# Optimization experiments

Measured on AMD Instinct MI355X. Metric: run time of the kernel, lower is better.

The kernel has to match this reference:

```python
import jax, jax.numpy as jnp
import numpy as np

S, B, D, N, DH = 2048, 2, 1024, 16, 64  # seq, batch, d_model, n_head, d_head
LN_EPS = 1e-5


def setup_inputs() -> dict:
    key = jax.random.key(0)
    ks = jax.random.split(key, 8)
    h = jax.random.normal(ks[0], (S, B, D), dtype=jnp.float32)
    Wq = jax.random.normal(ks[1], (D, N * DH), dtype=jnp.float32) * 0.02
    Wkv = jax.random.normal(ks[2], (D, 2 * N * DH), dtype=jnp.float32) * 0.02
    Wo = jax.random.normal(ks[3], (N * DH, D), dtype=jnp.float32) * 0.02
    ln_gamma = jnp.ones((D,), dtype=jnp.float32)
    ln_beta = jnp.zeros((D,), dtype=jnp.float32)
    # persistent compressive-memory state from a previous segment
    memory = jax.random.normal(ks[4], (B, N, DH, DH), dtype=jnp.float32)
    # normalization is a sum of (elu(k)+1) over ~S positions -> strictly positive, O(S)
    mem_norm = jax.random.uniform(ks[5], (B, 1, N, DH), dtype=jnp.float32) * S + 1.0
    gate_beta = jnp.ones((1,), dtype=jnp.float32) * 0.01  # beta_eps
    return {"h": h, "Wq": Wq, "Wkv": Wkv, "Wo": Wo, "ln_gamma": ln_gamma,
            "ln_beta": ln_beta, "memory": memory, "mem_norm": mem_norm,
            "gate_beta": gate_beta}


def reference(h, Wq, Wkv, Wo, ln_gamma, ln_beta, memory, mem_norm, gate_beta):
    scale = 1.0 / np.sqrt(DH).astype(np.float32)
    # projections (pre_lnorm=False, mems=None -> c == h)
    q = (h @ Wq).reshape(S, B, N, DH)
    k, v = jnp.split(h @ Wkv, 2, axis=-1)
    k = k.reshape(S, B, N, DH)
    v = v.reshape(S, B, N, DH)
    # local quadratic attention
    score = jnp.einsum('ibnd,jbnd->ijbn', q, k) * scale  # [S,S,B,N]
    prob = jax.nn.softmax(score, axis=1)
    attn_vec = jnp.einsum('ijbn,jbnd->ibnd', prob, v).reshape(S, B, N * DH)
    # memory retrieval (NOTE: source swaps K/V in the _update_memory call;
    # it is done under no_grad -> stop_gradient here)
    cached_Q = jax.nn.elu(q.swapaxes(0, 1)) + 1.0          # [B,S,N,DH]
    num = jnp.einsum('bsnk,bnkv->bsnv', cached_Q, memory)   # [B,S,N,DH]
    den = jnp.einsum('bsnk,bvnk->bsnv', cached_Q, mem_norm)  # [B,S,N,1]
    content_A = jax.lax.stop_gradient(num / den)            # [B,S,N,DH]
    # gated injection
    g = jax.nn.sigmoid(gate_beta)                           # [1]
    inj = g * content_A.swapaxes(0, 1).reshape(S, B, N * DH) + (1.0 - g) * attn_vec
    attn_out = inj @ Wo
    # post layernorm residual
    y = h + attn_out
    mu = jnp.mean(y, axis=-1, keepdims=True)
    var = jnp.mean((y - mu) ** 2, axis=-1, keepdims=True)
    return (y - mu) / jnp.sqrt(var + LN_EPS) * ln_gamma + ln_beta
```

## Files before the change

### kernel.cpp

```cpp
#include <hip/hip_runtime.h>


typedef unsigned short ushort_t;
typedef unsigned int uint32;

typedef __bf16 bf16x8 __attribute__((ext_vector_type(8)));
typedef float f32x4 __attribute__((ext_vector_type(4)));
typedef float f32x16 __attribute__((ext_vector_type(16)));
typedef unsigned short u16x8 __attribute__((ext_vector_type(8)));
typedef unsigned short u16x4 __attribute__((ext_vector_type(4)));
typedef unsigned int u32x4 __attribute__((ext_vector_type(4)));

typedef const __attribute__((address_space(1))) void gvoid_t;
typedef __attribute__((address_space(3))) void lvoid_t;

#define S_LEN 2048
#define BATCH 2
#define NHEAD 16

__device__ __forceinline__ ushort_t f2bf(float x) {
  union { float f; unsigned u; } c; c.f = x;
  unsigned r = (c.u + 0x7FFFu + ((c.u >> 16) & 1u)) >> 16;
  return (ushort_t)r;
}
__device__ __forceinline__ float bf2f(ushort_t v) {
  union { unsigned u; float f; } c; c.u = ((unsigned)v) << 16;
  return c.f;
}

__global__ __launch_bounds__(256) void k_cvt_h(const float* __restrict__ src,
                                               ushort_t* __restrict__ dst, int n4) {
  int idx = blockIdx.x * 256 + threadIdx.x;
  if (idx >= n4) return;
  float4 v = ((const float4*)src)[idx];
  u16x4 o; o[0] = f2bf(v.x); o[1] = f2bf(v.y); o[2] = f2bf(v.z); o[3] = f2bf(v.w);
  ((u16x4*)dst)[idx] = o;
}

__global__ __launch_bounds__(256) void k_cvt_wT(const float* __restrict__ W,
                                                ushort_t* __restrict__ WT, int K, int N) {
  __shared__ float tile[32][33];
  const int n0 = blockIdx.x * 32, k0 = blockIdx.y * 32;
  const int tx = threadIdx.x & 31, ty = threadIdx.x >> 5;
#pragma unroll
  for (int r = 0; r < 32; r += 8)
    tile[ty + r][tx] = W[(size_t)(k0 + ty + r) * N + n0 + tx];
  __syncthreads();
#pragma unroll
  for (int r = 0; r < 32; r += 8)
    WT[(size_t)(n0 + ty + r) * K + k0 + tx] = f2bf(tile[tx][ty + r]);
}

template <int OUT_BF16>
__global__ __launch_bounds__(256) void k_gemm_bt(const ushort_t* __restrict__ A,
                                                 const ushort_t* __restrict__ B,
                                                 void* __restrict__ Cv, int M, int N, int K,
                                                 int nbx) {
  __shared__ __attribute__((aligned(16))) ushort_t As[128 * 32];
  __shared__ __attribute__((aligned(16))) ushort_t Bs[128 * 32];
  const int per = gridDim.x >> 3;
  const int fl = (blockIdx.x & 7) * per + (blockIdx.x >> 3);
  const int m0 = (fl / nbx) * 128, n0 = (fl % nbx) * 128;
  const int tid = threadIdx.x, w = tid >> 6, lane = tid & 63;
  const int wm = (w >> 1) * 64, wn = (w & 1) * 64;
  const int l15 = lane & 15, l4 = lane >> 4;
  f32x4 acc[4][4];
#pragma unroll
  for (int i = 0; i < 4; ++i)
#pragma unroll
    for (int j = 0; j < 4; ++j)
#pragma unroll
      for (int r = 0; r < 4; ++r) acc[i][j][r] = 0.f;

  for (int k0 = 0; k0 < K; k0 += 32) {
    __syncthreads();
#pragma unroll
    for (int r = 0; r < 2; ++r) {
      int c = r * 256 + w * 64 + lane;
      const ushort_t* ga = A + (size_t)(m0 + (c >> 2)) * K + k0 + (c & 3) * 8;
      const ushort_t* gb = B + (size_t)(n0 + (c >> 2)) * K + k0 + (c & 3) * 8;
      __builtin_amdgcn_global_load_lds((gvoid_t*)ga, (lvoid_t*)(As + (r * 256 + w * 64) * 8), 16, 0, 0);
      __builtin_amdgcn_global_load_lds((gvoid_t*)gb, (lvoid_t*)(Bs + (r * 256 + w * 64) * 8), 16, 0, 0);
    }
    __syncthreads();
    bf16x8 af[4], bfr[4];
#pragma unroll
    for (int i = 0; i < 4; ++i) af[i] = *(const bf16x8*)&As[(wm + i * 16 + l15) * 32 + l4 * 8];
#pragma unroll
    for (int j = 0; j < 4; ++j) bfr[j] = *(const bf16x8*)&Bs[(wn + j * 16 + l15) * 32 + l4 * 8];
#pragma unroll
    for (int i = 0; i < 4; ++i)
#pragma unroll
      for (int j = 0; j < 4; ++j)
        acc[i][j] = __builtin_amdgcn_mfma_f32_16x16x32_bf16(af[i], bfr[j], acc[i][j], 0, 0, 0);
  }
#pragma unroll
  for (int i = 0; i < 4; ++i)
#pragma unroll
    for (int j = 0; j < 4; ++j)
#pragma unroll
      for (int r = 0; r < 4; ++r) {
        int row = m0 + wm + i * 16 + l4 * 4 + r;
        int col = n0 + wn + j * 16 + l15;
        if (OUT_BF16)
          ((ushort_t*)Cv)[(size_t)row * N + col] = f2bf(acc[i][j][r]);
        else
          ((float*)Cv)[(size_t)row * N + col] = acc[i][j][r];
      }
}

__device__ __forceinline__ void stage_k(const ushort_t* __restrict__ qkv, ushort_t* kw,
                                        int j0, int b, int n, int w, int lane) {
#pragma unroll
  for (int r = 0; r < 2; ++r) {
    int jb_ = w * 16 + r * 8;
    const ushort_t* ksrc = qkv + (size_t)(j0 + jb_ + (lane >> 3)) * 6144 + b * 3072 + n * 64 + 1024
                           + (((lane & 7) ^ (lane >> 3)) << 3);
    __builtin_amdgcn_global_load_lds((gvoid_t*)ksrc, (lvoid_t*)(kw + jb_ * 64), 16, 0, 0);
  }
}

__global__ __launch_bounds__(256) void k_attn(const ushort_t* __restrict__ qkv,
                                              const float* __restrict__ mem,
                                              const float* __restrict__ mnorm,
                                              const float* __restrict__ gbeta,
                                              ushort_t* __restrict__ inj) {
  __shared__ __attribute__((aligned(16))) ushort_t Ks[2][4096];
  __shared__ __attribute__((aligned(16))) ushort_t VTs[2][4096];
  __shared__ __attribute__((aligned(16))) ushort_t Ms[4096];
  const int bn = blockIdx.y, b = bn & 1, n = bn >> 1;
  const int tid = threadIdx.x, w = tid >> 6, lane = tid & 63;
  const int l31 = lane & 31, h = lane >> 5;
  const int qrow = blockIdx.x * 128 + w * 32 + l31;
  const size_t qoff = (size_t)qrow * 6144 + b * 3072 + n * 64;
  bf16x8 qf[4];
#pragma unroll
  for (int ks = 0; ks < 4; ++ks) qf[ks] = *(const bf16x8*)(qkv + qoff + ks * 16 + h * 8);

  const int vj = tid >> 2, vdq = (tid & 3) * 16, a2 = (tid & 3) * 2;
  const size_t vbase = (size_t)b * 3072 + n * 64 + 2048 + vdq;
  const int krd = l31 & 7;
  const int fv0 = (l31 & 7) ^ (l31 >> 3);
  const int fv1 = fv0 ^ 4;

  stage_k(qkv, Ks[0], 0, b, n, w, lane);
  u16x8 vr0 = *(const u16x8*)(qkv + (size_t)vj * 6144 + vbase);
  u16x8 vr1 = *(const u16x8*)(qkv + (size_t)vj * 6144 + vbase + 8);
  {
    const float* mb = mem + (size_t)(b * NHEAD + n) * 4096;
#pragma unroll
    for (int r = 0; r < 4; ++r) {
      float4 mv = *(const float4*)(mb + tid * 16 + r * 4);
      u16x4 mo;
      mo[0] = f2bf(mv.x); mo[1] = f2bf(mv.y); mo[2] = f2bf(mv.z); mo[3] = f2bf(mv.w);
      *(u16x4*)&Ms[tid * 16 + r * 4] = mo;
    }
  }
#pragma unroll
  for (int e = 0; e < 8; ++e) {
    int f0 = (e ^ a2) << 3;
    VTs[0][(vdq + e) * 64 + (vj ^ f0)] = vr0[e];
    VTs[0][(vdq + 8 + e) * 64 + (vj ^ f0 ^ 8)] = vr1[e];
  }
  __syncthreads();

  f32x16 oacc[2];
#pragma unroll
  for (int r = 0; r < 16; ++r) { oacc[0][r] = 0.f; oacc[1][r] = 0.f; }
  float m_run = -1e30f, l_run = 0.f;
  const float CEXP = 0.18033688011113723f;

  for (int t = 0; t < 32; ++t) {
    const ushort_t* Kb = Ks[t & 1];
    const ushort_t* Vb = VTs[t & 1];
    u16x8 nv0, nv1;
    if (t < 31) {
      stage_k(qkv, Ks[(t + 1) & 1], (t + 1) * 64, b, n, w, lane);
      const ushort_t* vsrc = qkv + (size_t)((t + 1) * 64 + vj) * 6144 + vbase;
      nv0 = *(const u16x8*)vsrc;
      nv1 = *(const u16x8*)(vsrc + 8);
    }
    f32x16 sv[2];
#pragma unroll
    for (int r = 0; r < 16; ++r) { sv[0][r] = 0.f; sv[1][r] = 0.f; }
    __builtin_amdgcn_s_setprio(1);
#pragma unroll
    for (int jb = 0; jb < 2; ++jb) {
      const int rb = (jb * 32 + l31) * 64;
#pragma unroll
      for (int ks = 0; ks < 4; ++ks) {
        bf16x8 kf = *(const bf16x8*)&Kb[rb + ((((ks << 1) | h) ^ krd) << 3)];
        sv[jb] = __builtin_amdgcn_mfma_f32_32x32x16_bf16(kf, qf[ks], sv[jb], 0, 0, 0);
      }
    }
    __builtin_amdgcn_s_setprio(0);
    float mx[16];
#pragma unroll
    for (int r = 0; r < 16; ++r) mx[r] = fmaxf(sv[0][r], sv[1][r]);
#pragma unroll
    for (int st = 8; st >= 1; st >>= 1)
#pragma unroll
      for (int r = 0; r < st; ++r) mx[r] = fmaxf(mx[r], mx[r + st]);
    float tmax = fmaxf(mx[0], __shfl_xor(mx[0], 32));
    if (!__all(tmax <= m_run + 60.0f)) {
      float mnew = fmaxf(m_run, tmax);
      float alpha = __builtin_amdgcn_exp2f((m_run - mnew) * CEXP);
      l_run *= alpha;
#pragma unroll
      for (int r = 0; r < 16; ++r) { oacc[0][r] *= alpha; oacc[1][r] *= alpha; }
      m_run = mnew;
    }
    float p[32];
    const float mc = m_run * CEXP;
#pragma unroll
    for (int jb = 0; jb < 2; ++jb)
#pragma unroll
      for (int r = 0; r < 16; ++r)
        p[jb * 16 + r] = __builtin_amdgcn_exp2f(fmaf(sv[jb][r], CEXP, -mc));
    float ls[16];
#pragma unroll
    for (int r = 0; r < 16; ++r) ls[r] = p[r] + p[16 + r];
#pragma unroll
    for (int st = 8; st >= 1; st >>= 1)
#pragma unroll
      for (int r = 0; r < st; ++r) ls[r] += ls[r + st];
    l_run += ls[0] + __shfl_xor(ls[0], 32);
#pragma unroll
    for (int ks = 0; ks < 4; ++ks) {
      const int jb = ks >> 1, q0 = (ks & 1) * 2;
      uint32 X0, X1, Y0, Y1;
      asm volatile("v_cvt_pk_bf16_f32 %0, %1, %2" : "=v"(X0) : "v"(p[jb * 16 + q0 * 4 + 0]), "v"(p[jb * 16 + q0 * 4 + 1]));
      asm volatile("v_cvt_pk_bf16_f32 %0, %1, %2" : "=v"(X1) : "v"(p[jb * 16 + q0 * 4 + 2]), "v"(p[jb * 16 + q0 * 4 + 3]));
      asm volatile("v_cvt_pk_bf16_f32 %0, %1, %2" : "=v"(Y0) : "v"(p[jb * 16 + (q0 + 1) * 4 + 0]), "v"(p[jb * 16 + (q0 + 1) * 4 + 1]));
      asm volatile("v_cvt_pk_bf16_f32 %0, %1, %2" : "=v"(Y1) : "v"(p[jb * 16 + (q0 + 1) * 4 + 2]), "v"(p[jb * 16 + (q0 + 1) * 4 + 3]));
      asm volatile("v_permlane32_swap_b32 %0, %1" : "+v"(X0), "+v"(Y0));
      asm volatile("v_permlane32_swap_b32 %0, %1" : "+v"(X1), "+v"(Y1));
      union { u32x4 u; bf16x8 v; } pf;
      pf.u[0] = X0; pf.u[1] = X1; pf.u[2] = Y0; pf.u[3] = Y1;
      bf16x8 vf0 = *(const bf16x8*)&Vb[l31 * 64 + ((((ks << 1) | h) ^ fv0) << 3)];
      bf16x8 vf1 = *(const bf16x8*)&Vb[(32 + l31) * 64 + ((((ks << 1) | h) ^ fv1) << 3)];
      __builtin_amdgcn_s_setprio(1);
      oacc[0] = __builtin_amdgcn_mfma_f32_32x32x16_bf16(vf0, pf.v, oacc[0], 0, 0, 0);
      oacc[1] = __builtin_amdgcn_mfma_f32_32x32x16_bf16(vf1, pf.v, oacc[1], 0, 0, 0);
      __builtin_amdgcn_s_setprio(0);
    }
    if (t < 31) {
      ushort_t* Vw = VTs[(t + 1) & 1];
#pragma unroll
      for (int e = 0; e < 8; ++e) {
        int f0 = (e ^ a2) << 3;
        Vw[(vdq + e) * 64 + (vj ^ f0)] = nv0[e];
        Vw[(vdq + 8 + e) * 64 + (vj ^ f0 ^ 8)] = nv1[e];
      }
      __syncthreads();
    }
  }

  float den = 0.f;
  bf16x8 cqf[4];
  const float* nrm = mnorm + (size_t)(b * NHEAD + n) * 64;
#pragma unroll
  for (int ks = 0; ks < 4; ++ks) {
    union { u16x8 u; bf16x8 v; } qv, cu;
    qv.v = qf[ks];
#pragma unroll
    for (int e = 0; e < 8; ++e) {
      float x = bf2f(qv.u[e]);
      float c = (x > 0.f) ? (x + 1.f) : __builtin_amdgcn_exp2f(x * 1.4426950408889634f);
      cu.u[e] = f2bf(c);
      den += c * nrm[ks * 16 + h * 8 + e];
    }
    cqf[ks] = cu.v;
  }
  den += __shfl_xor(den, 32);

  f32x16 accv[2];
#pragma unroll
  for (int r = 0; r < 16; ++r) { accv[0][r] = 0.f; accv[1][r] = 0.f; }
#pragma unroll
  for (int db = 0; db < 2; ++db)
#pragma unroll
    for (int ks = 0; ks < 4; ++ks) {
      union { u16x8 u; bf16x8 v; } af;
#pragma unroll
      for (int e = 0; e < 8; ++e)
        af.u[e] = Ms[(ks * 16 + h * 8 + e) * 64 + db * 32 + l31];
      accv[db] = __builtin_amdgcn_mfma_f32_32x32x16_bf16(af.v, cqf[ks], accv[db], 0, 0, 0);
    }

  float g = 1.f / (1.f + expf(-gbeta[0]));
  float rden = 1.f / den, invl = 1.f / l_run;
  ushort_t* op = inj + (size_t)qrow * 2048 + b * 1024 + n * 64;
#pragma unroll
  for (int db = 0; db < 2; ++db)
#pragma unroll
    for (int qq = 0; qq < 4; ++qq) {
      u16x4 st;
#pragma unroll
      for (int m = 0; m < 4; ++m) {
        float content = accv[db][qq * 4 + m] * rden;
        float av = oacc[db][qq * 4 + m] * invl;
        st[m] = f2bf(g * content + (1.f - g) * av);
      }
      *(u16x4*)(op + db * 32 + qq * 8 + h * 4) = st;
    }
}

__global__ __launch_bounds__(256) void k_ln(const float* __restrict__ h,
                                            const float* __restrict__ ao,
                                            const float* __restrict__ gam,
                                            const float* __restrict__ bet,
                                            float* __restrict__ out) {
  const int m = blockIdx.x, t = threadIdx.x;
  const int lane = t & 63, w = t >> 6;
  __shared__ float redS[4], redQ[4];
  const size_t base = (size_t)m * 1024;
  float4 hv = ((const float4*)(h + base))[t];
  float4 avv = ((const float4*)(ao + base))[t];
  float y0 = hv.x + avv.x, y1 = hv.y + avv.y, y2 = hv.z + avv.z, y3 = hv.w + avv.w;
  float s = y0 + y1 + y2 + y3;
  float sq = y0 * y0 + y1 * y1 + y2 * y2 + y3 * y3;
#pragma unroll
  for (int mk = 32; mk >= 1; mk >>= 1) { s += __shfl_xor(s, mk); sq += __shfl_xor(sq, mk); }
  if (lane == 0) { redS[w] = s; redQ[w] = sq; }
  __syncthreads();
  float Ssum = redS[0] + redS[1] + redS[2] + redS[3];
  float Qsum = redQ[0] + redQ[1] + redQ[2] + redQ[3];
  float mu = Ssum * (1.f / 1024.f);
  float var = Qsum * (1.f / 1024.f) - mu * mu;
  float rstd = rsqrtf(var + 1e-5f);
  float4 g = ((const float4*)gam)[t];
  float4 bt = ((const float4*)bet)[t];
  float4 o;
  o.x = (y0 - mu) * rstd * g.x + bt.x;
  o.y = (y1 - mu) * rstd * g.y + bt.y;
  o.z = (y2 - mu) * rstd * g.z + bt.z;
  o.w = (y3 - mu) * rstd * g.w + bt.w;
  ((float4*)(out + base))[t] = o;
}

extern "C" void kernel_launch(void* const* d_in, const int* in_sizes, int n_in,
                              void* d_out, int out_size, void* d_ws, size_t ws_size,
                              hipStream_t stream) {
  const float* h = (const float*)d_in[0];
  const float* Wq = (const float*)d_in[1];
  const float* Wkv = (const float*)d_in[2];
  const float* Wo = (const float*)d_in[3];
  const float* gam = (const float*)d_in[4];
  const float* bet = (const float*)d_in[5];
  const float* mem = (const float*)d_in[6];
  const float* mnorm = (const float*)d_in[7];
  const float* gbeta = (const float*)d_in[8];
  float* out = (float*)d_out;

  char* ws = (char*)d_ws;
  ushort_t* hb  = (ushort_t*)(ws);
  ushort_t* wT  = (ushort_t*)(ws + (size_t)(8u << 20));
  ushort_t* woT = (ushort_t*)(ws + (size_t)(14u << 20));
  ushort_t* qkv = (ushort_t*)(ws + (size_t)(16u << 20));
  float*    ao  = (float*)   (ws + (size_t)(16u << 20));
  ushort_t* inj = hb;

  k_cvt_h<<<4096, 256, 0, stream>>>(h, hb, 1048576);
  k_cvt_wT<<<dim3(32, 32), 256, 0, stream>>>(Wq, wT, 1024, 1024);
  k_cvt_wT<<<dim3(64, 32), 256, 0, stream>>>(Wkv, wT + (size_t)1024 * 1024, 1024, 2048);
  k_cvt_wT<<<dim3(32, 32), 256, 0, stream>>>(Wo, woT, 1024, 1024);
  k_gemm_bt<1><<<768, 256, 0, stream>>>(hb, wT, (void*)qkv, 4096, 3072, 1024, 24);
  k_attn<<<dim3(16, 32), 256, 0, stream>>>(qkv, mem, mnorm, gbeta, inj);
  k_gemm_bt<0><<<256, 256, 0, stream>>>(inj, woT, (void*)ao, 4096, 1024, 1024, 8);
  k_ln<<<4096, 256, 0, stream>>>(h, ao, gam, bet, out);
}
```

Before: 155.8 us.

## Split attention KV range across two half-blocks and add 64-row output GEMM

The attention kernel now runs 512 threads per block. Each half processes 16 of the 32 key tiles, and the two partial softmax states are merged through shared memory, which doubles parallelism across the key dimension. The memory matrix is no longer staged in LDS; it is read straight from global memory and converted in the retrieval MFMA loop. The output projection moves to a new GEMM with 64x128 tiles and 512 blocks for better CU coverage. In exchange there is extra LDS traffic for the merge, idle threads in the upper half after the merge, and uncoalesced global reads of the memory matrix.

After: 169.2 us. +8.5%, slower.

```diff
diff --git a/kernel.cpp b/kernel.cpp
--- a/kernel.cpp
+++ b/kernel.cpp
@@ -109,6 +109,60 @@
       }
 }
 
+__global__ __launch_bounds__(256) void k_gemm64(const ushort_t* __restrict__ A,
+                                                const ushort_t* __restrict__ B,
+                                                float* __restrict__ C, int M, int N, int K,
+                                                int nbx) {
+  __shared__ __attribute__((aligned(16))) ushort_t As[64 * 32];
+  __shared__ __attribute__((aligned(16))) ushort_t Bs[128 * 32];
+  const int per = gridDim.x >> 3;
+  const int fl = (blockIdx.x & 7) * per + (blockIdx.x >> 3);
+  const int m0 = (fl / nbx) * 64, n0 = (fl % nbx) * 128;
+  const int tid = threadIdx.x, w = tid >> 6, lane = tid & 63;
+  const int wn = w * 32;
+  const int l15 = lane & 15, l4 = lane >> 4;
+  f32x4 acc[4][2];
+#pragma unroll
+  for (int i = 0; i < 4; ++i)
+#pragma unroll
+    for (int j = 0; j < 2; ++j)
+#pragma unroll
+      for (int r = 0; r < 4; ++r) acc[i][j][r] = 0.f;
+
+  for (int k0 = 0; k0 < K; k0 += 32) {
+    __syncthreads();
+    {
+      int c = w * 64 + lane;
+      const ushort_t* ga = A + (size_t)(m0 + (c >> 2)) * K + k0 + (c & 3) * 8;
+      __builtin_amdgcn_global_load_lds((gvoid_t*)ga, (lvoid_t*)(As + w * 512), 16, 0, 0);
+#pragma unroll
+      for (int r = 0; r < 2; ++r) {
+        int c2 = r * 256 + w * 64 + lane;
+        const ushort_t* gb = B + (size_t)(n0 + (c2 >> 2)) * K + k0 + (c2 & 3) * 8;
+        __builtin_amdgcn_global_load_lds((gvoid_t*)gb, (lvoid_t*)(Bs + r * 2048 + w * 512), 16, 0, 0);
+      }
+    }
+    __syncthreads();
+    bf16x8 af[4], bfr[2];
+#pragma unroll
+    for (int i = 0; i < 4; ++i) af[i] = *(const bf16x8*)&As[(i * 16 + l15) * 32 + l4 * 8];
+#pragma unroll
+    for (int j = 0; j < 2; ++j) bfr[j] = *(const bf16x8*)&Bs[(wn + j * 16 + l15) * 32 + l4 * 8];
+#pragma unroll
+    for (int i = 0; i < 4; ++i)
+#pragma unroll
+      for (int j = 0; j < 2; ++j)
+        acc[i][j] = __builtin_amdgcn_mfma_f32_16x16x32_bf16(af[i], bfr[j], acc[i][j], 0, 0, 0);
+  }
+#pragma unroll
+  for (int i = 0; i < 4; ++i)
+#pragma unroll
+    for (int j = 0; j < 2; ++j)
+#pragma unroll
+      for (int r = 0; r < 4; ++r)
+        C[(size_t)(m0 + i * 16 + l4 * 4 + r) * N + n0 + wn + j * 16 + l15] = acc[i][j][r];
+}
+
 __device__ __forceinline__ void stage_k(const ushort_t* __restrict__ qkv, ushort_t* kw,
                                         int j0, int b, int n, int w, int lane) {
 #pragma unroll
@@ -120,47 +174,43 @@
   }
 }
 
-__global__ __launch_bounds__(256) void k_attn(const ushort_t* __restrict__ qkv,
-                                              const float* __restrict__ mem,
-                                              const float* __restrict__ mnorm,
-                                              const float* __restrict__ gbeta,
-                                              ushort_t* __restrict__ inj) {
-  __shared__ __attribute__((aligned(16))) ushort_t Ks[2][4096];
-  __shared__ __attribute__((aligned(16))) ushort_t VTs[2][4096];
-  __shared__ __attribute__((aligned(16))) ushort_t Ms[4096];
+__global__ __launch_bounds__(512, 4) void k_attn(const ushort_t* __restrict__ qkv,
+                                                 const float* __restrict__ mem,
+                                                 const float* __restrict__ mnorm,
+                                                 const float* __restrict__ gbeta,
+                                                 ushort_t* __restrict__ inj) {
+  __shared__ __attribute__((aligned(16))) ushort_t smem[32768];
   const int bn = blockIdx.y, b = bn & 1, n = bn >> 1;
-  const int tid = threadIdx.x, w = tid >> 6, lane = tid & 63;
+  const int tid = threadIdx.x;
+  const int hh = tid >> 8;
+  const int ht = tid & 255;
+  const int w4 = (tid >> 6) & 3, lane = tid & 63;
   const int l31 = lane & 31, h = lane >> 5;
-  const int qrow = blockIdx.x * 128 + w * 32 + l31;
+  const int qrow = blockIdx.x * 128 + w4 * 32 + l31;
   const size_t qoff = (size_t)qrow * 6144 + b * 3072 + n * 64;
   bf16x8 qf[4];
 #pragma unroll
   for (int ks = 0; ks < 4; ++ks) qf[ks] = *(const bf16x8*)(qkv + qoff + ks * 16 + h * 8);
 
-  const int vj = tid >> 2, vdq = (tid & 3) * 16, a2 = (tid & 3) * 2;
+  const int vj = ht >> 2, vdq = (ht & 3) * 16, a2 = (ht & 3) * 2;
   const size_t vbase = (size_t)b * 3072 + n * 64 + 2048 + vdq;
   const int krd = l31 & 7;
   const int fv0 = (l31 & 7) ^ (l31 >> 3);
   const int fv1 = fv0 ^ 4;
-
-  stage_k(qkv, Ks[0], 0, b, n, w, lane);
-  u16x8 vr0 = *(const u16x8*)(qkv + (size_t)vj * 6144 + vbase);
-  u16x8 vr1 = *(const u16x8*)(qkv + (size_t)vj * 6144 + vbase + 8);
+  const int tile0 = hh * 16;
+
+  stage_k(qkv, smem + hh * 8192, tile0 * 64, b, n, w4, lane);
   {
-    const float* mb = mem + (size_t)(b * NHEAD + n) * 4096;
-#pragma unroll
-    for (int r = 0; r < 4; ++r) {
-      float4 mv = *(const float4*)(mb + tid * 16 + r * 4);
-      u16x4 mo;
-      mo[0] = f2bf(mv.x); mo[1] = f2bf(mv.y); mo[2] = f2bf(mv.z); mo[3] = f2bf(mv.w);
-      *(u16x4*)&Ms[tid * 16 + r * 4] = mo;
-    }
-  }
-#pragma unroll
-  for (int e = 0; e < 8; ++e) {
-    int f0 = (e ^ a2) << 3;
-    VTs[0][(vdq + e) * 64 + (vj ^ f0)] = vr0[e];
-    VTs[0][(vdq + 8 + e) * 64 + (vj ^ f0 ^ 8)] = vr1[e];
+    const ushort_t* vsrc = qkv + (size_t)(tile0 * 64 + vj) * 6144 + vbase;
+    u16x8 vr0 = *(const u16x8*)vsrc;
+    u16x8 vr1 = *(const u16x8*)(vsrc + 8);
+    ushort_t* Vw = smem + 16384 + hh * 8192;
+#pragma unroll
+    for (int e = 0; e < 8; ++e) {
+      int f0 = (e ^ a2) << 3;
+      Vw[(vdq + e) * 64 + (vj ^ f0)] = vr0[e];
+      Vw[(vdq + 8 + e) * 64 + (vj ^ f0 ^ 8)] = vr1[e];
+    }
   }
   __syncthreads();
 
@@ -170,13 +220,14 @@
   float m_run = -1e30f, l_run = 0.f;
   const float CEXP = 0.18033688011113723f;
 
-  for (int t = 0; t < 32; ++t) {
-    const ushort_t* Kb = Ks[t & 1];
-    const ushort_t* Vb = VTs[t & 1];
+  for (int t = 0; t < 16; ++t) {
+    const int bb = t & 1;
+    const ushort_t* Kb = smem + (hh * 2 + bb) * 4096;
+    const ushort_t* Vb = smem + 16384 + (hh * 2 + bb) * 4096;
     u16x8 nv0, nv1;
-    if (t < 31) {
-      stage_k(qkv, Ks[(t + 1) & 1], (t + 1) * 64, b, n, w, lane);
-      const ushort_t* vsrc = qkv + (size_t)((t + 1) * 64 + vj) * 6144 + vbase;
+    if (t < 15) {
+      stage_k(qkv, smem + (hh * 2 + (bb ^ 1)) * 4096, (tile0 + t + 1) * 64, b, n, w4, lane);
+      const ushort_t* vsrc = qkv + (size_t)((tile0 + t + 1) * 64 + vj) * 6144 + vbase;
       nv0 = *(const u16x8*)vsrc;
       nv1 = *(const u16x8*)(vsrc + 8);
     }
@@ -244,8 +295,8 @@
       oacc[1] = __builtin_amdgcn_mfma_f32_32x32x16_bf16(vf1, pf.v, oacc[1], 0, 0, 0);
       __builtin_amdgcn_s_setprio(0);
     }
-    if (t < 31) {
-      ushort_t* Vw = VTs[(t + 1) & 1];
+    if (t < 15) {
+      ushort_t* Vw = smem + 16384 + (hh * 2 + (bb ^ 1)) * 4096;
 #pragma unroll
       for (int e = 0; e < 8; ++e) {
         int f0 = (e ^ a2) << 3;
@@ -256,6 +307,37 @@
     }
   }
 
+  __syncthreads();
+  float* exO = (float*)smem;
+  float* exml = (float*)(smem + 16384);
+  if (hh == 1) {
+    float* eo = exO + (w4 * 64 + lane) * 32;
+#pragma unroll
+    for (int r = 0; r < 16; ++r) {
+      eo[(r + lane) & 31] = oacc[0][r];
+      eo[(16 + r + lane) & 31] = oacc[1][r];
+    }
+    exml[(w4 * 64 + lane) * 2] = m_run;
+    exml[(w4 * 64 + lane) * 2 + 1] = l_run;
+  }
+  __syncthreads();
+  if (hh == 1) return;
+
+  {
+    const float* eo = exO + (w4 * 64 + lane) * 32;
+    float m1 = exml[(w4 * 64 + lane) * 2];
+    float l1 = exml[(w4 * 64 + lane) * 2 + 1];
+    float mnew = fmaxf(m_run, m1);
+    float a0 = __builtin_amdgcn_exp2f((m_run - mnew) * CEXP);
+    float a1 = __builtin_amdgcn_exp2f((m1 - mnew) * CEXP);
+    l_run = l_run * a0 + l1 * a1;
+#pragma unroll
+    for (int r = 0; r < 16; ++r) {
+      oacc[0][r] = oacc[0][r] * a0 + eo[(r + lane) & 31] * a1;
+      oacc[1][r] = oacc[1][r] * a0 + eo[(16 + r + lane) & 31] * a1;
+    }
+  }
+
   float den = 0.f;
   bf16x8 cqf[4];
   const float* nrm = mnorm + (size_t)(b * NHEAD + n) * 64;
@@ -274,6 +356,7 @@
   }
   den += __shfl_xor(den, 32);
 
+  const float* mb = mem + (size_t)(b * NHEAD + n) * 4096;
   f32x16 accv[2];
 #pragma unroll
   for (int r = 0; r < 16; ++r) { accv[0][r] = 0.f; accv[1][r] = 0.f; }
@@ -284,7 +367,7 @@
       union { u16x8 u; bf16x8 v; } af;
 #pragma unroll
       for (int e = 0; e < 8; ++e)
-        af.u[e] = Ms[(ks * 16 + h * 8 + e) * 64 + db * 32 + l31];
+        af.u[e] = f2bf(mb[(size_t)(ks * 16 + h * 8 + e) * 64 + db * 32 + l31]);
       accv[db] = __builtin_amdgcn_mfma_f32_32x32x16_bf16(af.v, cqf[ks], accv[db], 0, 0, 0);
     }
 
@@ -366,7 +449,7 @@
   k_cvt_wT<<<dim3(64, 32), 256, 0, stream>>>(Wkv, wT + (size_t)1024 * 1024, 1024, 2048);
   k_cvt_wT<<<dim3(32, 32), 256, 0, stream>>>(Wo, woT, 1024, 1024);
   k_gemm_bt<1><<<768, 256, 0, stream>>>(hb, wT, (void*)qkv, 4096, 3072, 1024, 24);
-  k_attn<<<dim3(16, 32), 256, 0, stream>>>(qkv, mem, mnorm, gbeta, inj);
-  k_gemm_bt<0><<<256, 256, 0, stream>>>(inj, woT, (void*)ao, 4096, 1024, 1024, 8);
+  k_attn<<<dim3(16, 32), 512, 0, stream>>>(qkv, mem, mnorm, gbeta, inj);
+  k_gemm64<<<512, 256, 0, stream>>>(inj, woT, ao, 4096, 1024, 1024, 8);
   k_ln<<<4096, 256, 0, stream>>>(h, ao, gam, bet, out);
 }
```
